# Optimization experiments

Measured on AMD Instinct MI355X. Metric: run time of the kernel, lower is better.

The kernel has to match this reference:

```python
import jax, jax.numpy as jnp
import numpy as np

N, M = 3000, 6000            # nodes, edges
FV, FE, H1, H2, NC = 128, 64, 256, 128, 16


def setup_inputs() -> dict:
    key = jax.random.key(0)
    ks = jax.random.split(key, 20)
    r = lambda i, sh: jax.random.normal(ks[i], sh, dtype=jnp.float32)
    return dict(
        X=r(0, (N, FV)),
        Z=r(1, (M, FE)),
        adj_e=jax.random.uniform(ks[2], (M, M), dtype=jnp.float32),
        adj_v=jax.random.uniform(ks[3], (N, N), dtype=jnp.float32),
        T=jax.random.uniform(ks[4], (N, M), dtype=jnp.float32),
        edge_index=jax.random.randint(ks[5], (2, 2 * M), 0, N),
        W1=r(6, (FV, H1)) * 0.05, b1=jnp.zeros((H1,), jnp.float32),
        p2=r(7, (1, H1)), W2=r(8, (FE, FE)) * 0.05, b2=jnp.zeros((FE,), jnp.float32),
        p3=r(9, (1, H1)), W3=r(10, (FE, FE)) * 0.05, b3=jnp.zeros((FE,), jnp.float32),
        p32=r(11, (1, H1)), W32=r(12, (FE, FE)) * 0.05, b32=jnp.zeros((FE,), jnp.float32),
        p4=r(13, (1, FE)), W4=r(14, (H1, H2)) * 0.05,
        b4g=jnp.zeros((H2,), jnp.float32), b4=jnp.zeros((H2,), jnp.float32),
        W5=r(15, (H2, NC)) * 0.05, b5=jnp.zeros((NC,), jnp.float32),
    )


def gcn(x, W, b, edge_index, n):
    """PyG GCNConv: symmetric-normalized A+I propagation."""
    src, dst = edge_index[0], edge_index[1]
    loop = jnp.arange(n)
    s = jnp.concatenate([src, loop])
    d = jnp.concatenate([dst, loop])
    deg = jax.ops.segment_sum(jnp.ones(s.shape[0], x.dtype), d, num_segments=n)
    dinv = jnp.where(deg > 0, jax.lax.rsqrt(deg), 0.0)
    norm = dinv[s] * dinv[d]                      # [E+n]
    xw = x @ W                                    # [n, out]
    return jax.ops.segment_sum(xw[s] * norm[:, None], d, num_segments=n) + b


def edge_layer(Hv, He, adj_e, T, p, W, b):
    # multiplier2 = T.T @ diag(Hv @ p.T) @ T, done as a fused column scale of T
    sv = (Hv @ p.T)[:, 0]                         # [n]
    m2 = T.T @ (T * sv[:, None])                  # [m, m]
    idx = jnp.arange(m2.shape[0])
    M3 = m2.at[idx, idx].set(1.0)                 # identity on diag, m2 off-diag
    A = M3 * adj_e
    An = A / A.max(axis=0, keepdims=True)         # column-max normalize
    return An @ (He @ W) + b


def reference(X, Z, adj_e, adj_v, T, edge_index,
              W1, b1, p2, W2, b2, p3, W3, b3, p32, W32, b32,
              p4, W4, b4g, b4, W5, b5):
    relu = jax.nn.relu
    # gc1: plain GCN on nodes (normalGCN=True), edges passed through
    Xh = relu(gcn(X, W1, b1, edge_index, N))
    Zh = relu(Z)
    # gc2, gc3, gc3_2: edge layers
    Zh = relu(edge_layer(Xh, Zh, adj_e, T, p2, W2, b2)); Xh = relu(Xh)
    Zh = relu(edge_layer(Xh, Zh, adj_e, T, p3, W3, b3)); Xh = relu(Xh)
    Zh = relu(edge_layer(Xh, Zh, adj_e, T, p32, W32, b32)); Xh = relu(Xh)
    # gc4: node layer with multiplier1 = T @ diag(He @ p.T) @ T.T
    se = (Zh @ p4.T)[:, 0]                        # [m]
    mult1 = (T * se[None, :]) @ T.T               # [n, n]
    X4 = mult1 @ gcn(Xh, W4, b4g, edge_index, N) + b4
    Xh = relu(X4); Zh = relu(Zh)
    # gc5: plain GCN -> softmax over classes
    X5 = gcn(Xh, W5, b5, edge_index, N)
    return jax.nn.softmax(X5, axis=1)
```

## Files before the change

### kernel.cpp

```cpp
#include <hip/hip_runtime.h>
#include <cmath>
#include <cstddef>

#define NN 3000
#define MM 6000
#define FV 128
#define FE 64
#define H1 256
#define H2 128
#define NC 16
#define E2 12000

#define CT_E 47
#define CTA_E 48
#define KT_E 94
#define CT_M 24
#define KT_M 188
#define KT_A 188
#define NPK_M 94
#define PKA_BYTES ((size_t)CTA_E * KT_E * 8192)
#define PKM_BYTES ((size_t)CT_M * KT_M * 8192)
#define APK_BYTES ((size_t)CT_E * KT_A * 8192)

static inline int cdiv(int a, int b) { return (a + b - 1) / b; }

typedef __attribute__((ext_vector_type(8))) short short8;
typedef __attribute__((ext_vector_type(4))) float f32x4;

__device__ inline void atomicMaxFloat(float* addr, float v) {
  if (v >= 0.f) atomicMax((int*)addr, __float_as_int(v));
  else          atomicMin((unsigned int*)addr, __float_as_uint(v));
}

__device__ inline unsigned short b2h(float x) {
  unsigned int u = __float_as_uint(x);
  return (unsigned short)((u + 0x7FFFu + ((u >> 16) & 1u)) >> 16);
}

__device__ inline void bsplit(float x, unsigned short& h, unsigned short& l) {
  h = b2h(x);
  float hf = __uint_as_float(((unsigned int)h) << 16);
  l = b2h(x - hf);
}

__global__ void k_fill(float* p, float v, int n) {
  int i = blockIdx.x * blockDim.x + threadIdx.x;
  if (i < n) p[i] = v;
}

__global__ void k_fill_bias(float* p, const float* __restrict__ bias, int nmask, int total) {
  int i = blockIdx.x * blockDim.x + threadIdx.x;
  if (i < total) p[i] = bias[i & nmask];
}

__global__ void k_relu_copy(const float* __restrict__ in, float* __restrict__ out, int n) {
  int i = blockIdx.x * blockDim.x + threadIdx.x;
  if (i < n) out[i] = fmaxf(in[i], 0.f);
}

__global__ void k_relu(float* p, int n) {
  int i = blockIdx.x * blockDim.x + threadIdx.x;
  if (i < n) p[i] = fmaxf(p[i], 0.f);
}

__global__ void k_deg_count(const int* __restrict__ dst, float* deg, int ne) {
  int e = blockIdx.x * blockDim.x + threadIdx.x;
  if (e < ne) atomicAdd(&deg[dst[e]], 1.f);
}

__global__ void k_dinv(float* deg, int n) {
  int i = blockIdx.x * blockDim.x + threadIdx.x;
  if (i < n) deg[i] = rsqrtf(deg[i] + 1.0f);
}

__global__ void k_gcn_init(const float* __restrict__ xw, const float* __restrict__ dinv,
                           const float* __restrict__ bias, float* __restrict__ out,
                           int n, int flog2) {
  int idx = blockIdx.x * blockDim.x + threadIdx.x;
  int F = 1 << flog2;
  if (idx < n * F) {
    int i = idx >> flog2;
    int f = idx & (F - 1);
    float di = dinv[i];
    out[idx] = xw[idx] * di * di + bias[f];
  }
}

__global__ void k_gcn_scatter(const float* __restrict__ xw, const int* __restrict__ src,
                              const int* __restrict__ dst, const float* __restrict__ dinv,
                              float* __restrict__ out, int ne, int flog2) {
  int idx = blockIdx.x * blockDim.x + threadIdx.x;
  int F = 1 << flog2;
  if (idx < ne * F) {
    int e = idx >> flog2;
    int f = idx & (F - 1);
    int s = src[e], d = dst[e];
    atomicAdd(&out[d * F + f], xw[s * F + f] * dinv[s] * dinv[d]);
  }
}

__global__ void k_rowdot(const float* __restrict__ Xv, const float* __restrict__ p,
                         float* __restrict__ out, int rows, int K) {
  int row = blockIdx.x * 4 + (threadIdx.x >> 6);
  int lane = threadIdx.x & 63;
  if (row >= rows) return;
  float acc = 0.f;
  for (int k = lane; k < K; k += 64) acc += Xv[(size_t)row * K + k] * p[k];
  for (int off = 32; off > 0; off >>= 1) acc += __shfl_xor(acc, off);
  if (lane == 0) out[row] = acc;
}

__global__ void k_prep(const float* __restrict__ HeW, const float* __restrict__ cmax,
                       const float* __restrict__ bias,
                       float* __restrict__ Bc, float* __restrict__ Zh, int total) {
  int idx = blockIdx.x * blockDim.x + threadIdx.x;
  if (idx < total) {
    Bc[idx] = HeW[idx] / cmax[idx >> 6];
    Zh[idx] = bias[idx & 63];
  }
}

__global__ void k_prep_pack(const float* __restrict__ HeW, const float* __restrict__ cmax,
                            const float* __restrict__ bias,
                            float* __restrict__ Zh, char* __restrict__ Bpk, int Kd) {
  int kt = blockIdx.x;
  int t = threadIdx.x;
  int f = t >> 2, g = t & 3;
  float bf = bias[f];
  unsigned short hv[8];
#pragma unroll
  for (int e = 0; e < 8; ++e) {
    int k = kt * 32 + g * 8 + e;
    float v = 0.f;
    if (k < Kd) {
      v = HeW[(size_t)k * 64 + f] / cmax[k];
      Zh[(size_t)k * 64 + f] = bf;
    }
    hv[e] = b2h(v);
  }
  uint4 H;
  H.x = (unsigned)hv[0] | ((unsigned)hv[1] << 16);
  H.y = (unsigned)hv[2] | ((unsigned)hv[3] << 16);
  H.z = (unsigned)hv[4] | ((unsigned)hv[5] << 16);
  H.w = (unsigned)hv[6] | ((unsigned)hv[7] << 16);
  *(uint4*)(Bpk + (size_t)kt * 4096 + f * 64 + ((g ^ ((f >> 1) & 3)) * 16)) = H;
}

__global__ void k_pack_g(const float* __restrict__ g, char* __restrict__ gpk, int Kd) {
  int kt = blockIdx.x;
  int t = threadIdx.x;
#pragma unroll
  for (int it = 0; it < 2; ++it) {
    int idx = it * 256 + t;
    int f = idx >> 2, gsw = idx & 3;
    int gq = gsw ^ ((f >> 1) & 3);
    unsigned short hv[8];
#pragma unroll
    for (int e = 0; e < 8; ++e) {
      int k = kt * 32 + gq * 8 + e;
      float v = (k < Kd) ? g[(size_t)k * 128 + f] : 0.f;
      hv[e] = b2h(v);
    }
    uint4 H;
    H.x = (unsigned)hv[0] | ((unsigned)hv[1] << 16);
    H.y = (unsigned)hv[2] | ((unsigned)hv[3] << 16);
    H.z = (unsigned)hv[4] | ((unsigned)hv[5] << 16);
    H.w = (unsigned)hv[6] | ((unsigned)hv[7] << 16);
    *(uint4*)(gpk + (size_t)kt * 8192 + idx * 16) = H;
  }
}

__global__ void k_scale_pack(const char* __restrict__ src, char* __restrict__ dst,
                             const float* __restrict__ s, float* __restrict__ cmax,
                             int nkt, int nk, int Md) {
  int ct = blockIdx.x, kt = blockIdx.y;
  size_t base = ((size_t)ct * nkt + kt) * 8192;
  int t = threadIdx.x;
  if (cmax && kt == 0 && t < 128) {
    int cc = ct * 128 + t;
    if (cc < Md) cmax[cc] = -INFINITY;
  }
#pragma unroll
  for (int it = 0; it < 2; ++it) {
    int idx = it * 256 + t;
    int c = idx >> 2, gsw = idx & 3;
    int g = gsw ^ ((c >> 1) & 3);
    uint4 H = *(const uint4*)(src + base + idx * 16);
    unsigned int hw[4] = {H.x, H.y, H.z, H.w};
    unsigned int ow[4];
#pragma unroll
    for (int p = 0; p < 4; ++p) {
      int k0 = kt * 32 + g * 8 + p * 2;
      float s0 = (k0 < nk) ? s[k0] : 0.f;
      float s1 = (k0 + 1 < nk) ? s[k0 + 1] : 0.f;
      float v0 = __uint_as_float((hw[p] & 0xFFFFu) << 16) * s0;
      float v1 = __uint_as_float((hw[p] >> 16) << 16) * s1;
      ow[p] = (unsigned)b2h(v0) | ((unsigned)b2h(v1) << 16);
    }
    uint4 O;
    O.x = ow[0]; O.y = ow[1]; O.z = ow[2]; O.w = ow[3];
    *(uint4*)(dst + base + idx * 16) = O;
  }
}

__global__ void k_pack_edge(const float* __restrict__ T, const float* __restrict__ svp,
                            char* __restrict__ ph, char* __restrict__ pl,
                            float* __restrict__ cmax,
                            int scaled, int Md, int Kd, int nkt) {
  int ct = blockIdx.x, kt = blockIdx.y;
  size_t base = ((size_t)ct * nkt + kt) * 8192;
  int t = threadIdx.x;
  if (scaled && kt == 0 && t < 128) {
    int cc = ct * 128 + t;
    if (cc < Md) cmax[cc] = -INFINITY;
  }
#pragma unroll
  for (int it = 0; it < 2; ++it) {
    int tau = it * 256 + t;
    int c = tau & 127;
    int g = tau >> 7;
    int gc = ct * 128 + c;
    int off = c * 64 + ((g ^ ((c >> 1) & 3)) * 16);
    unsigned short hv[8], lv[8];
#pragma unroll
    for (int e = 0; e < 8; ++e) {
      int k = kt * 32 + g * 8 + e;
      float v = 0.f;
      if (k < Kd && gc < Md) {
        v = T[(size_t)k * Md + gc];
        if (scaled) v *= svp[k];
      }
      bsplit(v, hv[e], lv[e]);
    }
    uint4 H, L;
    H.x = (unsigned)hv[0] | ((unsigned)hv[1] << 16);
    H.y = (unsigned)hv[2] | ((unsigned)hv[3] << 16);
    H.z = (unsigned)hv[4] | ((unsigned)hv[5] << 16);
    H.w = (unsigned)hv[6] | ((unsigned)hv[7] << 16);
    *(uint4*)(ph + base + off) = H;
    if (pl) {
      L.x = (unsigned)lv[0] | ((unsigned)lv[1] << 16);
      L.y = (unsigned)lv[2] | ((unsigned)lv[3] << 16);
      L.z = (unsigned)lv[4] | ((unsigned)lv[5] << 16);
      L.w = (unsigned)lv[6] | ((unsigned)lv[7] << 16);
      *(uint4*)(pl + base + off) = L;
    }
  }
}

__global__ void k_pack_tt(const float* __restrict__ T, const float* __restrict__ sep,
                          char* __restrict__ ph, char* __restrict__ pl,
                          int scaled, int Mt, int Kt, int nkt) {
  int ct = blockIdx.x, kt = blockIdx.y;
  size_t base = ((size_t)ct * nkt + kt) * 8192;
  int t = threadIdx.x;
#pragma unroll
  for (int it = 0; it < 2; ++it) {
    int tau = it * 256 + t;
    int c = tau >> 2;
    int g = tau & 3;
    int node = ct * 128 + c;
    int off = c * 64 + ((g ^ ((c >> 1) & 3)) * 16);
    unsigned short hv[8], lv[8];
#pragma unroll
    for (int e = 0; e < 8; ++e) {
      int k = kt * 32 + g * 8 + e;
      float v = 0.f;
      if (node < Mt && k < Kt) {
        v = T[(size_t)node * Kt + k];
        if (scaled) v *= sep[k];
      }
      bsplit(v, hv[e], lv[e]);
    }
    uint4 H, L;
    H.x = (unsigned)hv[0] | ((unsigned)hv[1] << 16);
    H.y = (unsigned)hv[2] | ((unsigned)hv[3] << 16);
    H.z = (unsigned)hv[4] | ((unsigned)hv[5] << 16);
    H.w = (unsigned)hv[6] | ((unsigned)hv[7] << 16);
    *(uint4*)(ph + base + off) = H;
    if (pl) {
      L.x = (unsigned)lv[0] | ((unsigned)lv[1] << 16);
      L.y = (unsigned)lv[2] | ((unsigned)lv[3] << 16);
      L.z = (unsigned)lv[4] | ((unsigned)lv[5] << 16);
      L.w = (unsigned)lv[6] | ((unsigned)lv[7] << 16);
      *(uint4*)(pl + base + off) = L;
    }
  }
}

template <int EPI>
__global__ __launch_bounds__(512) void k_tsvt_pk(const char* __restrict__ pAh,
                                                 const char* __restrict__ pBh,
                                                 const float* __restrict__ adj,
                                                 char* __restrict__ Opk,
                                                 float* __restrict__ cmax,
                                                 int Md, int nkt, int nbtI, int nbtJ,
                                                 int npk) {
  __shared__ __align__(16) char smem[49152];
  const int tid = threadIdx.x;
  const int lane = tid & 63;
  const int w = tid >> 6;
  const int wr = w >> 1;
  const int wc = w & 1;
  const int r16 = lane & 15;
  const int kb = lane >> 4;

  int nwg = nbtI * nbtJ;
  int orig = blockIdx.x;
  int q = nwg >> 3, r = nwg & 7;
  int xcd = orig & 7, pos = orig >> 3;
  int wgid = (xcd < r ? xcd * (q + 1) : r * (q + 1) + (xcd - r) * q) + pos;
  int gpb = 8 * nbtJ;
  int g0 = wgid / gpb;
  int rem = wgid - g0 * gpb;
  int gh = nbtI - g0 * 8; if (gh > 8) gh = 8;
  int bj = rem / gh;
  int bi = g0 * 8 + (rem - bj * gh);

  const int i0 = bi * 256, j0 = bj * 128;

  const char* srcb[3];
  srcb[0] = pAh + ((size_t)(2 * bi) * nkt) * 8192;
  srcb[1] = pAh + ((size_t)(2 * bi + 1) * nkt) * 8192;
  srcb[2] = pBh + ((size_t)bj * nkt) * 8192;
  const int woff = w * 1024 + lane * 16;

  auto stage = [&](int kt, int buf) {
#pragma unroll
    for (int rnd = 0; rnd < 3; ++rnd) {
      const char* s = srcb[rnd] + (size_t)kt * 8192 + woff;
      __builtin_amdgcn_global_load_lds(
          (const __attribute__((address_space(1))) void*)s,
          (__attribute__((address_space(3))) void*)(smem + buf * 24576 + rnd * 8192 + woff),
          16, 0, 0);
    }
  };

  f32x4 acc[4][4];
#pragma unroll
  for (int a = 0; a < 4; ++a)
#pragma unroll
    for (int b = 0; b < 4; ++b) acc[a][b] = 0.f;

  stage(0, 0);
  __syncthreads();
  int cur = 0;
  for (int kt = 0; kt < nkt; ++kt) {
    if (kt + 1 < nkt) stage(kt + 1, cur ^ 1);
    const char* sA = smem + cur * 24576;
    const char* sB = sA + 16384;

    short8 bh[4];
#pragma unroll
    for (int nj = 0; nj < 4; ++nj) {
      int col = wc * 64 + nj * 16 + r16;
      bh[nj] = *(const short8*)(sB + col * 64 + ((kb ^ ((col >> 1) & 3)) * 16));
    }
#pragma unroll
    for (int mi = 0; mi < 4; ++mi) {
      int row = wr * 64 + mi * 16 + r16;
      int off = (row >> 7) * 8192 + (row & 127) * 64 + ((kb ^ ((row >> 1) & 3)) * 16);
      short8 ah = *(const short8*)(sA + off);
#pragma unroll
      for (int nj = 0; nj < 4; ++nj)
        acc[mi][nj] = __builtin_amdgcn_mfma_f32_16x16x32_bf16(ah, bh[nj], acc[mi][nj], 0, 0, 0);
    }
    __syncthreads();
    cur ^= 1;
  }

#pragma unroll
  for (int nj = 0; nj < 4; ++nj) {
    int j = j0 + wc * 64 + nj * 16 + r16;
    float cm = -INFINITY;
    bool jok = (j < Md);
#pragma unroll
    for (int mi = 0; mi < 4; ++mi) {
      int ib = i0 + wr * 64 + mi * 16 + kb * 4;
      f32x4 a = acc[mi][nj];
#pragma unroll
      for (int r = 0; r < 4; ++r) {
        int i = ib + r;
        if (i < Md && jok) {
          float v = a[r];
          if (EPI == 1) {
            if (i == j) v = 1.0f;
            v *= __builtin_nontemporal_load(&adj[(size_t)i * Md + j]);
            cm = fmaxf(cm, v);
          }
          *(unsigned short*)(Opk + ((size_t)(i >> 7) * npk + (j >> 5)) * 8192
              + (i & 127) * 64 + ((((j >> 3) & 3) ^ ((i >> 1) & 3)) * 16) + (j & 7) * 2)
              = b2h(v);
        }
      }
    }
    if (EPI == 1) {
      cm = fmaxf(cm, __shfl_xor(cm, 16));
      cm = fmaxf(cm, __shfl_xor(cm, 32));
      if (kb == 0 && jok) atomicMaxFloat(&cmax[j], cm);
    }
  }
}

__global__ __launch_bounds__(256) void k_zh(const char* __restrict__ Apk,
                                            const char* __restrict__ Bpk,
                                            float* __restrict__ Zh,
                                            int Mn, int nktA, int zchunk) {
  __shared__ __align__(16) char smem[12288];
  const int tid = threadIdx.x;
  const int lane = tid & 63;
  const int w = tid >> 6;
  const int r16 = lane & 15;
  const int kb = lane >> 4;
  const int bi = blockIdx.x;
  const int kt0 = blockIdx.y * zchunk;
  const int kt1 = min(nktA, kt0 + zchunk);
  const int i0 = bi * 128;

  f32x4 acc[2][4];
#pragma unroll
  for (int a = 0; a < 2; ++a)
#pragma unroll
    for (int b = 0; b < 4; ++b) acc[a][b] = 0.f;

  for (int kt = kt0; kt < kt1; ++kt) {
    const char* As = Apk + ((size_t)bi * nktA + kt) * 8192;
    const char* Bs = Bpk + (size_t)kt * 4096;
    __builtin_amdgcn_global_load_lds(
        (const __attribute__((address_space(1))) void*)(As + tid * 16),
        (__attribute__((address_space(3))) void*)(smem + tid * 16), 16, 0, 0);
    __builtin_amdgcn_global_load_lds(
        (const __attribute__((address_space(1))) void*)(As + 4096 + tid * 16),
        (__attribute__((address_space(3))) void*)(smem + 4096 + tid * 16), 16, 0, 0);
    __builtin_amdgcn_global_load_lds(
        (const __attribute__((address_space(1))) void*)(Bs + tid * 16),
        (__attribute__((address_space(3))) void*)(smem + 8192 + tid * 16), 16, 0, 0);
    __syncthreads();
    short8 bh[4];
#pragma unroll
    for (int nj = 0; nj < 4; ++nj) {
      int f = nj * 16 + r16;
      bh[nj] = *(const short8*)(smem + 8192 + f * 64 + ((kb ^ ((f >> 1) & 3)) * 16));
    }
#pragma unroll
    for (int mi = 0; mi < 2; ++mi) {
      int c = w * 32 + mi * 16 + r16;
      short8 ah = *(const short8*)(smem + c * 64 + ((kb ^ ((c >> 1) & 3)) * 16));
#pragma unroll
      for (int nj = 0; nj < 4; ++nj)
        acc[mi][nj] = __builtin_amdgcn_mfma_f32_16x16x32_bf16(ah, bh[nj], acc[mi][nj], 0, 0, 0);
    }
    __syncthreads();
  }
#pragma unroll
  for (int mi = 0; mi < 2; ++mi) {
    int ib = i0 + w * 32 + mi * 16 + kb * 4;
#pragma unroll
    for (int nj = 0; nj < 4; ++nj) {
      int f = nj * 16 + r16;
      f32x4 a = acc[mi][nj];
#pragma unroll
      for (int r = 0; r < 4; ++r) {
        int i = ib + r;
        if (i < Mn) atomicAdd(&Zh[(size_t)i * 64 + f], a[r]);
      }
    }
  }
}

__global__ __launch_bounds__(256) void k_zh128(const char* __restrict__ Apk,
                                               const char* __restrict__ Bpk,
                                               float* __restrict__ C,
                                               int Mn, int nktA, int zchunk) {
  __shared__ __align__(16) char smem[16384];
  const int tid = threadIdx.x;
  const int lane = tid & 63;
  const int w = tid >> 6;
  const int r16 = lane & 15;
  const int kb = lane >> 4;
  const int bi = blockIdx.x;
  const int kt0 = blockIdx.y * zchunk;
  const int kt1 = min(nktA, kt0 + zchunk);
  const int i0 = bi * 128;

  f32x4 acc[2][8];
#pragma unroll
  for (int a = 0; a < 2; ++a)
#pragma unroll
    for (int b = 0; b < 8; ++b) acc[a][b] = 0.f;

  for (int kt = kt0; kt < kt1; ++kt) {
    const char* As = Apk + ((size_t)bi * nktA + kt) * 8192;
    const char* Bs = Bpk + (size_t)kt * 8192;
#pragma unroll
    for (int o = 0; o < 4; ++o) {
      int idx = o * 256 + tid;
      const char* s = (idx < 512) ? (As + idx * 16) : (Bs + (idx - 512) * 16);
      __builtin_amdgcn_global_load_lds(
          (const __attribute__((address_space(1))) void*)s,
          (__attribute__((address_space(3))) void*)(smem + idx * 16), 16, 0, 0);
    }
    __syncthreads();
    short8 bh[8];
#pragma unroll
    for (int nj = 0; nj < 8; ++nj) {
      int f = nj * 16 + r16;
      bh[nj] = *(const short8*)(smem + 8192 + f * 64 + ((kb ^ ((f >> 1) & 3)) * 16));
    }
#pragma unroll
    for (int mi = 0; mi < 2; ++mi) {
      int c = w * 32 + mi * 16 + r16;
      short8 ah = *(const short8*)(smem + c * 64 + ((kb ^ ((c >> 1) & 3)) * 16));
#pragma unroll
      for (int nj = 0; nj < 8; ++nj)
        acc[mi][nj] = __builtin_amdgcn_mfma_f32_16x16x32_bf16(ah, bh[nj], acc[mi][nj], 0, 0, 0);
    }
    __syncthreads();
  }
#pragma unroll
  for (int mi = 0; mi < 2; ++mi) {
    int ib = i0 + w * 32 + mi * 16 + kb * 4;
#pragma unroll
    for (int nj = 0; nj < 8; ++nj) {
      int f = nj * 16 + r16;
      f32x4 a = acc[mi][nj];
#pragma unroll
      for (int r = 0; r < 4; ++r) {
        int i = ib + r;
        if (i < Mn) atomicAdd(&C[(size_t)i * 128 + f], a[r]);
      }
    }
  }
}

template <int EPI>
__global__ __launch_bounds__(256) void k_tsvt_cvt(const float* __restrict__ Tmat,
                                                  const float* __restrict__ svp,
                                                  const float* __restrict__ adj,
                                                  float* __restrict__ Out,
                                                  float* __restrict__ cmax,
                                                  int Md, int Kd) {
  __shared__ __align__(16) unsigned short sAh[128 * 32];
  __shared__ __align__(16) unsigned short sAl[128 * 32];
  __shared__ __align__(16) unsigned short sBh[128 * 32];
  __shared__ __align__(16) unsigned short sBl[128 * 32];
  const int tid = threadIdx.x;
  const int lane = tid & 63;
  const int w = tid >> 6;
  const int wr = w >> 1, wc = w & 1;
  const int r16 = lane & 15;
  const int kb = lane >> 4;
  const int i0 = blockIdx.y * 128;
  const int j0 = blockIdx.x * 128;
  f32x4 acc[4][4];
#pragma unroll
  for (int a = 0; a < 4; ++a)
#pragma unroll
    for (int b = 0; b < 4; ++b) acc[a][b] = 0.f;
  for (int k0 = 0; k0 < Kd; k0 += 32) {
#pragma unroll
    for (int it = 0; it < 4; ++it) {
      int s = tid + it * 256;
      int ci = s & 127;
      int kq = s >> 7;
      int kk = kq * 4;
      int kbq = kq >> 1, half = kq & 1;
      int off = ci * 64 + (kbq ^ ((ci >> 1) & 3)) * 16 + half * 8;
      float va[4];
#pragma unroll
      for (int e = 0; e < 4; ++e) {
        int k = k0 + kk + e;
        int c = i0 + ci;
        va[e] = (k < Kd && c < Md) ? Tmat[(size_t)k * Md + c] : 0.f;
      }
      unsigned short h0, h1, h2, h3, l0, l1, l2, l3;
      bsplit(va[0], h0, l0); bsplit(va[1], h1, l1);
      bsplit(va[2], h2, l2); bsplit(va[3], h3, l3);
      uint2 hp, lp;
      hp.x = (unsigned)h0 | ((unsigned)h1 << 16); hp.y = (unsigned)h2 | ((unsigned)h3 << 16);
      lp.x = (unsigned)l0 | ((unsigned)l1 << 16); lp.y = (unsigned)l2 | ((unsigned)l3 << 16);
      *(uint2*)((char*)sAh + off) = hp;
      *(uint2*)((char*)sAl + off) = lp;
      float vb[4];
#pragma unroll
      for (int e = 0; e < 4; ++e) {
        int k = k0 + kk + e;
        int c = j0 + ci;
        float svv = (k < Kd) ? svp[k] : 0.f;
        vb[e] = (k < Kd && c < Md) ? Tmat[(size_t)k * Md + c] * svv : 0.f;
      }
      bsplit(vb[0], h0, l0); bsplit(vb[1], h1, l1);
      bsplit(vb[2], h2, l2); bsplit(vb[3], h3, l3);
      hp.x = (unsigned)h0 | ((unsigned)h1 << 16); hp.y = (unsigned)h2 | ((unsigned)h3 << 16);
      lp.x = (unsigned)l0 | ((unsigned)l1 << 16); lp.y = (unsigned)l2 | ((unsigned)l3 << 16);
      *(uint2*)((char*)sBh + off) = hp;
      *(uint2*)((char*)sBl + off) = lp;
    }
    __syncthreads();
    short8 bh[4], bl[4];
#pragma unroll
    for (int nj = 0; nj < 4; ++nj) {
      int col = wc * 64 + nj * 16 + r16;
      int off = col * 64 + ((kb ^ ((col >> 1) & 3)) * 16);
      bh[nj] = *(const short8*)((const char*)sBh + off);
      bl[nj] = *(const short8*)((const char*)sBl + off);
    }
#pragma unroll
    for (int mi = 0; mi < 4; ++mi) {
      int row = wr * 64 + mi * 16 + r16;
      int off = row * 64 + ((kb ^ ((row >> 1) & 3)) * 16);
      short8 ah = *(const short8*)((const char*)sAh + off);
      short8 al = *(const short8*)((const char*)sAl + off);
#pragma unroll
      for (int nj = 0; nj < 4; ++nj) {
        acc[mi][nj] = __builtin_amdgcn_mfma_f32_16x16x32_bf16(ah, bh[nj], acc[mi][nj], 0, 0, 0);
        acc[mi][nj] = __builtin_amdgcn_mfma_f32_16x16x32_bf16(ah, bl[nj], acc[mi][nj], 0, 0, 0);
        acc[mi][nj] = __builtin_amdgcn_mfma_f32_16x16x32_bf16(al, bh[nj], acc[mi][nj], 0, 0, 0);
      }
    }
    __syncthreads();
  }
#pragma unroll
  for (int nj = 0; nj < 4; ++nj) {
    int j = j0 + wc * 64 + nj * 16 + r16;
    float cm = -INFINITY;
#pragma unroll
    for (int mi = 0; mi < 4; ++mi) {
      int ib = i0 + wr * 64 + mi * 16 + kb * 4;
      f32x4 a = acc[mi][nj];
#pragma unroll
      for (int r = 0; r < 4; ++r) {
        int i = ib + r;
        if (i < Md && j < Md) {
          float v = a[r];
          if (EPI == 1) {
            if (i == j) v = 1.0f;
            v *= adj[(size_t)i * Md + j];
            Out[(size_t)i * Md + j] = v;
            cm = fmaxf(cm, v);
          } else {
            Out[(size_t)i * Md + j] = v;
          }
        }
      }
    }
    if (EPI == 1) {
      cm = fmaxf(cm, __shfl_xor(cm, 16));
      cm = fmaxf(cm, __shfl_xor(cm, 32));
      if (kb == 0 && j < Md) atomicMaxFloat(&cmax[j], cm);
    }
  }
}

template <int SPLITK, int NT>
__global__ __launch_bounds__(256) void k_gemm64(const float* __restrict__ Am,
                                                const float* __restrict__ Bm,
                                                const float* __restrict__ bias,
                                                const float* __restrict__ kscale,
                                                float* __restrict__ C,
                                                int Mn, int Nn, int Kn, int relu) {
  __shared__ float As[16][68];
  __shared__ float Bs[16][68];
  int i0 = blockIdx.y * 64, j0 = blockIdx.x * 64;
  int kchunk = (Kn + SPLITK - 1) / SPLITK;
  int ks = blockIdx.z * kchunk;
  int ke = min(Kn, ks + kchunk);
  int tid = threadIdx.x;
  int tx = tid & 15, ty = tid >> 4;
  float acc[4][4] = {};
  for (int k0 = ks; k0 < ke; k0 += 16) {
#pragma unroll
    for (int l0 = 0; l0 < 1024; l0 += 256) {
      int l = l0 + tid;
      int i = l >> 4, k = l & 15;
      float v = 0.f;
      if (i0 + i < Mn && k0 + k < ke) {
        v = NT ? __builtin_nontemporal_load(&Am[(size_t)(i0 + i) * Kn + (k0 + k)])
               : Am[(size_t)(i0 + i) * Kn + (k0 + k)];
        if (kscale) v *= kscale[k0 + k];
      }
      As[k][i] = v;
    }
#pragma unroll
    for (int l0 = 0; l0 < 1024; l0 += 256) {
      int l = l0 + tid;
      int k = l >> 6, j = l & 63;
      float v = 0.f;
      if (k0 + k < ke && j0 + j < Nn) v = Bm[(size_t)(k0 + k) * Nn + (j0 + j)];
      Bs[k][j] = v;
    }
    __syncthreads();
#pragma unroll
    for (int k = 0; k < 16; ++k) {
      const float4 av = *(const float4*)&As[k][ty * 4];
      const float4 bv = *(const float4*)&Bs[k][tx * 4];
      float a_[4] = {av.x, av.y, av.z, av.w};
      float b_[4] = {bv.x, bv.y, bv.z, bv.w};
#pragma unroll
      for (int ri = 0; ri < 4; ++ri)
#pragma unroll
        for (int rj = 0; rj < 4; ++rj)
          acc[ri][rj] = fmaf(a_[ri], b_[rj], acc[ri][rj]);
    }
    __syncthreads();
  }
#pragma unroll
  for (int ri = 0; ri < 4; ++ri) {
    int i = i0 + ty * 4 + ri;
    if (i >= Mn) continue;
#pragma unroll
    for (int rj = 0; rj < 4; ++rj) {
      int j = j0 + tx * 4 + rj;
      if (j >= Nn) continue;
      float v = acc[ri][rj];
      if (SPLITK > 1) {
        atomicAdd(&C[(size_t)i * Nn + j], v);
      } else {
        if (bias) v += bias[j];
        if (relu) v = fmaxf(v, 0.f);
        C[(size_t)i * Nn + j] = v;
      }
    }
  }
}

__global__ void k_transpose(const float* __restrict__ in, float* __restrict__ out,
                            int rows, int cols) {
  __shared__ float tile[32][33];
  int c0 = blockIdx.x * 32, r0 = blockIdx.y * 32;
  int tx = threadIdx.x & 31, tg = threadIdx.x >> 5;
  for (int rr = tg; rr < 32; rr += 8) {
    int r = r0 + rr, c = c0 + tx;
    tile[rr][tx] = (r < rows && c < cols) ? in[(size_t)r * cols + c] : 0.f;
  }
  __syncthreads();
  for (int rr = tg; rr < 32; rr += 8) {
    int c = c0 + rr, r = r0 + tx;
    if (c < cols && r < rows) out[(size_t)c * rows + r] = tile[tx][rr];
  }
}

__global__ void k_softmax16(const float* __restrict__ X5, float* __restrict__ out, int rows) {
  int r = blockIdx.x * blockDim.x + threadIdx.x;
  if (r >= rows) return;
  float v[16];
  float m = -INFINITY;
#pragma unroll
  for (int c = 0; c < 16; ++c) { v[c] = X5[r * 16 + c]; m = fmaxf(m, v[c]); }
  float s = 0.f;
#pragma unroll
  for (int c = 0; c < 16; ++c) { v[c] = expf(v[c] - m); s += v[c]; }
  float inv = 1.f / s;
#pragma unroll
  for (int c = 0; c < 16; ++c) out[r * 16 + c] = v[c] * inv;
}

extern "C" void kernel_launch(void* const* d_in, const int* in_sizes, int n_in,
                              void* d_out, int out_size, void* d_ws, size_t ws_size,
                              hipStream_t stream) {
  const float* X     = (const float*)d_in[0];
  const float* Z     = (const float*)d_in[1];
  const float* adj_e = (const float*)d_in[2];
  const float* Tm    = (const float*)d_in[4];
  const int*   ei    = (const int*)d_in[5];
  const int* src = ei;
  const int* dst = ei + E2;
  const float* W1  = (const float*)d_in[6];
  const float* b1  = (const float*)d_in[7];
  const float* p2  = (const float*)d_in[8];
  const float* W2  = (const float*)d_in[9];
  const float* b2  = (const float*)d_in[10];
  const float* p3  = (const float*)d_in[11];
  const float* W3  = (const float*)d_in[12];
  const float* b3  = (const float*)d_in[13];
  const float* p32 = (const float*)d_in[14];
  const float* W32 = (const float*)d_in[15];
  const float* b32 = (const float*)d_in[16];
  const float* p4  = (const float*)d_in[17];
  const float* W4  = (const float*)d_in[18];
  const float* b4g = (const float*)d_in[19];
  const float* b4  = (const float*)d_in[20];
  const float* W5  = (const float*)d_in[21];
  const float* b5  = (const float*)d_in[22];

  char* wsb = (char*)d_ws;
  const bool big = ws_size >= (size_t)310 * 1024 * 1024;

  char* Apk  = wsb;
  char* pAhi = wsb + APK_BYTES;
  char* pBhi = pAhi + PKA_BYTES;
  char* Bpk  = wsb + 145539072;
  char* mAhi = wsb;
  char* mBhi = mAhi + PKM_BYTES;
  char* Mpk  = wsb + 80000000;
  char* gpk  = wsb + 100000000;

  float* small = big ? (float*)(wsb + 182000000) : (float*)d_ws + 36000000;
  float* Xh   = small;
  float* xw   = small + 768000;
  float* Zh   = small + 1536000;
  float* HeW  = small + 1920000;
  float* Bc   = small + 2304000;
  float* g    = small + 2688000;
  float* sv   = small + 3072000;
  float* se   = small + 3076096;
  float* cmax = small + 3084288;
  float* dinv = small + 3090432;
  float* X5   = small + 3093504;
  float* A_fb     = (float*)d_ws;
  float* Tt_fb    = (float*)d_ws;
  float* mult1_fb = (float*)d_ws + 18000000;
  float* out  = (float*)d_out;

  auto gemm = [&](const float* Am, const float* Bm, const float* bias, const float* ksc,
                  float* C, int Mn, int Nn, int Kn, int relu, int splitk, int nt) {
    dim3 gr(cdiv(Nn, 64), cdiv(Mn, 64), splitk);
    if (splitk == 1) {
      if (nt) k_gemm64<1, 1><<<gr, 256, 0, stream>>>(Am, Bm, bias, ksc, C, Mn, Nn, Kn, relu);
      else    k_gemm64<1, 0><<<gr, 256, 0, stream>>>(Am, Bm, bias, ksc, C, Mn, Nn, Kn, relu);
    } else {
      if (nt) k_gemm64<4, 1><<<gr, 256, 0, stream>>>(Am, Bm, bias, ksc, C, Mn, Nn, Kn, relu);
      else    k_gemm64<4, 0><<<gr, 256, 0, stream>>>(Am, Bm, bias, ksc, C, Mn, Nn, Kn, relu);
    }
  };

  k_fill<<<cdiv(NN, 256), 256, 0, stream>>>(dinv, 0.f, NN);
  k_deg_count<<<cdiv(E2, 256), 256, 0, stream>>>(dst, dinv, E2);
  k_dinv<<<cdiv(NN, 256), 256, 0, stream>>>(dinv, NN);

  gemm(X, W1, nullptr, nullptr, xw, NN, H1, FV, 0, 1, 0);
  k_gcn_init<<<cdiv(NN * H1, 256), 256, 0, stream>>>(xw, dinv, b1, Xh, NN, 8);
  k_gcn_scatter<<<cdiv(E2 * H1, 256), 256, 0, stream>>>(xw, src, dst, dinv, Xh, E2, 8);
  k_relu<<<cdiv(NN * H1, 256), 256, 0, stream>>>(Xh, NN * H1);
  k_relu_copy<<<cdiv(MM * FE, 256), 256, 0, stream>>>(Z, Zh, MM * FE);

  if (big) {
    dim3 gp(CTA_E, KT_E);
    k_pack_edge<<<gp, 256, 0, stream>>>(Tm, nullptr, pAhi, nullptr, nullptr, 0, MM, NN, KT_E);
  }

  const float* ep[3] = {p2, p3, p32};
  const float* eW[3] = {W2, W3, W32};
  const float* eb[3] = {b2, b3, b32};
  for (int L = 0; L < 3; ++L) {
    k_rowdot<<<cdiv(NN, 4), 256, 0, stream>>>(Xh, ep[L], sv, NN, H1);
    gemm(Zh, eW[L], nullptr, nullptr, HeW, MM, FE, FE, 0, 1, 0);
    if (big) {
      dim3 gs(CT_E, KT_E);
      k_scale_pack<<<gs, 256, 0, stream>>>(pAhi, pBhi, sv, cmax, KT_E, NN, MM);
      int nbtI = cdiv(MM, 256), nbtJ = CT_E;
      k_tsvt_pk<1><<<nbtI * nbtJ, 512, 0, stream>>>(pAhi, pBhi, adj_e, Apk, cmax,
                                                    MM, KT_E, nbtI, nbtJ, KT_A);
      k_prep_pack<<<KT_A, 256, 0, stream>>>(HeW, cmax, eb[L], Zh, Bpk, MM);
      dim3 gz(CT_E, 8);
      k_zh<<<gz, 256, 0, stream>>>(Apk, Bpk, Zh, MM, KT_A, cdiv(KT_A, 8));
    } else {
      k_fill<<<cdiv(MM, 256), 256, 0, stream>>>(cmax, -INFINITY, MM);
      dim3 gm2(CT_E, CT_E);
      k_tsvt_cvt<1><<<gm2, 256, 0, stream>>>(Tm, sv, adj_e, A_fb, cmax, MM, NN);
      k_prep<<<cdiv(MM * FE, 256), 256, 0, stream>>>(HeW, cmax, eb[L], Bc, Zh, MM * FE);
      gemm(A_fb, Bc, nullptr, nullptr, Zh, MM, FE, MM, 0, 4, 1);
    }
    k_relu<<<cdiv(MM * FE, 256), 256, 0, stream>>>(Zh, MM * FE);
  }

  k_rowdot<<<cdiv(MM, 4), 256, 0, stream>>>(Zh, p4, se, MM, FE);
  gemm(Xh, W4, nullptr, nullptr, xw, NN, H2, H1, 0, 1, 0);
  k_gcn_init<<<cdiv(NN * H2, 256), 256, 0, stream>>>(xw, dinv, b4g, g, NN, 7);
  k_gcn_scatter<<<cdiv(E2 * H2, 256), 256, 0, stream>>>(xw, src, dst, dinv, g, E2, 7);
  if (big) {
    dim3 gp(CT_M, KT_M);
    k_pack_tt<<<gp, 256, 0, stream>>>(Tm, nullptr, mAhi, nullptr, 0, NN, MM, KT_M);
    dim3 gs(CT_M, KT_M);
    k_scale_pack<<<gs, 256, 0, stream>>>(mAhi, mBhi, se, nullptr, KT_M, MM, 0);
    int nbtI = cdiv(NN, 256), nbtJ = cdiv(NN, 128);
    k_tsvt_pk<0><<<nbtI * nbtJ, 512, 0, stream>>>(mAhi, mBhi, nullptr, Mpk, nullptr,
                                                  NN, KT_M, nbtI, nbtJ, NPK_M);
    k_pack_g<<<NPK_M, 256, 0, stream>>>(g, gpk, NN);
    k_fill_bias<<<cdiv(NN * H2, 256), 256, 0, stream>>>(Xh, b4, H2 - 1, NN * H2);
    dim3 gx(CT_M, 8);
    k_zh128<<<gx, 256, 0, stream>>>(Mpk, gpk, Xh, NN, NPK_M, cdiv(NPK_M, 8));
  } else {
    dim3 gt(cdiv(MM, 32), cdiv(NN, 32));
    k_transpose<<<gt, 256, 0, stream>>>(Tm, Tt_fb, NN, MM);
    dim3 gm1(cdiv(NN, 128), cdiv(NN, 128));
    k_tsvt_cvt<0><<<gm1, 256, 0, stream>>>(Tt_fb, se, nullptr, mult1_fb, nullptr, NN, MM);
    k_fill_bias<<<cdiv(NN * H2, 256), 256, 0, stream>>>(Xh, b4, H2 - 1, NN * H2);
    gemm(mult1_fb, g, nullptr, nullptr, Xh, NN, H2, NN, 0, 4, 0);
  }
  k_relu<<<cdiv(NN * H2, 256), 256, 0, stream>>>(Xh, NN * H2);

  gemm(Xh, W5, nullptr, nullptr, xw, NN, NC, H2, 0, 1, 0);
  k_gcn_init<<<cdiv(NN * NC, 256), 256, 0, stream>>>(xw, dinv, b5, X5, NN, 4);
  k_gcn_scatter<<<cdiv(E2 * NC, 256), 256, 0, stream>>>(xw, src, dst, dinv, X5, E2, 4);
  k_softmax16<<<cdiv(NN, 256), 256, 0, stream>>>(X5, out, NN);
}
```

Measured before the change: 1.421 ms.

## Exploit symmetry of T^T diag(s) T by computing only upper-triangular tiles

Measured after the change: 1.376 ms. 1.03x faster.

```diff
diff --git a/kernel.cpp b/kernel.cpp
--- a/kernel.cpp
+++ b/kernel.cpp
@@ -12,13 +12,12 @@
 #define E2 12000
 
 #define CT_E 47
-#define CTA_E 48
 #define KT_E 94
 #define CT_M 24
 #define KT_M 188
 #define KT_A 188
 #define NPK_M 94
-#define PKA_BYTES ((size_t)CTA_E * KT_E * 8192)
+#define PKA_BYTES ((size_t)48 * KT_E * 8192)
 #define PKM_BYTES ((size_t)CT_M * KT_M * 8192)
 #define APK_BYTES ((size_t)CT_E * KT_A * 8192)
 
@@ -289,14 +288,13 @@
 }
 
 template <int EPI>
-__global__ __launch_bounds__(512) void k_tsvt_pk(const char* __restrict__ pAh,
-                                                 const char* __restrict__ pBh,
-                                                 const float* __restrict__ adj,
-                                                 char* __restrict__ Opk,
-                                                 float* __restrict__ cmax,
-                                                 int Md, int nkt, int nbtI, int nbtJ,
-                                                 int npk) {
-  __shared__ __align__(16) char smem[49152];
+__global__ __launch_bounds__(256) void k_tsvt_sym(const char* __restrict__ pAh,
+                                                  const char* __restrict__ pBh,
+                                                  const float* __restrict__ adj,
+                                                  char* __restrict__ Opk,
+                                                  float* __restrict__ cmax,
+                                                  int Md, int nkt, int nbt, int npk) {
+  __shared__ __align__(16) char smem[32768];
   const int tid = threadIdx.x;
   const int lane = tid & 63;
   const int w = tid >> 6;
@@ -305,33 +303,30 @@
   const int r16 = lane & 15;
   const int kb = lane >> 4;
 
-  int nwg = nbtI * nbtJ;
+  int nwg = nbt * (nbt + 1) / 2;
   int orig = blockIdx.x;
   int q = nwg >> 3, r = nwg & 7;
   int xcd = orig & 7, pos = orig >> 3;
   int wgid = (xcd < r ? xcd * (q + 1) : r * (q + 1) + (xcd - r) * q) + pos;
-  int gpb = 8 * nbtJ;
-  int g0 = wgid / gpb;
-  int rem = wgid - g0 * gpb;
-  int gh = nbtI - g0 * 8; if (gh > 8) gh = 8;
-  int bj = rem / gh;
-  int bi = g0 * 8 + (rem - bj * gh);
-
-  const int i0 = bi * 256, j0 = bj * 128;
-
-  const char* srcb[3];
-  srcb[0] = pAh + ((size_t)(2 * bi) * nkt) * 8192;
-  srcb[1] = pAh + ((size_t)(2 * bi + 1) * nkt) * 8192;
-  srcb[2] = pBh + ((size_t)bj * nkt) * 8192;
-  const int woff = w * 1024 + lane * 16;
+  int bi = 0, rem = wgid;
+  while (rem >= nbt - bi) { rem -= nbt - bi; ++bi; }
+  int bj = bi + rem;
+
+  const int i0 = bi * 128, j0 = bj * 128;
+
+  const char* srcA = pAh + (size_t)bi * nkt * 8192;
+  const char* srcB = pBh + (size_t)bj * nkt * 8192;
+  const int c4 = w * 4;
 
   auto stage = [&](int kt, int buf) {
 #pragma unroll
-    for (int rnd = 0; rnd < 3; ++rnd) {
-      const char* s = srcb[rnd] + (size_t)kt * 8192 + woff;
+    for (int o = 0; o < 4; ++o) {
+      int c = c4 + o;
+      int sel = c >> 3, sub = c & 7;
+      const char* s = (sel ? srcB : srcA) + (size_t)kt * 8192 + sub * 1024 + lane * 16;
       __builtin_amdgcn_global_load_lds(
           (const __attribute__((address_space(1))) void*)s,
-          (__attribute__((address_space(3))) void*)(smem + buf * 24576 + rnd * 8192 + woff),
+          (__attribute__((address_space(3))) void*)(smem + buf * 16384 + c * 1024 + lane * 16),
           16, 0, 0);
     }
   };
@@ -347,8 +342,8 @@
   int cur = 0;
   for (int kt = 0; kt < nkt; ++kt) {
     if (kt + 1 < nkt) stage(kt + 1, cur ^ 1);
-    const char* sA = smem + cur * 24576;
-    const char* sB = sA + 16384;
+    const char* sA = smem + cur * 16384;
+    const char* sB = sA + 8192;
 
     short8 bh[4];
 #pragma unroll
@@ -359,8 +354,7 @@
 #pragma unroll
     for (int mi = 0; mi < 4; ++mi) {
       int row = wr * 64 + mi * 16 + r16;
-      int off = (row >> 7) * 8192 + (row & 127) * 64 + ((kb ^ ((row >> 1) & 3)) * 16);
-      short8 ah = *(const short8*)(sA + off);
+      short8 ah = *(const short8*)(sA + row * 64 + ((kb ^ ((row >> 1) & 3)) * 16));
 #pragma unroll
       for (int nj = 0; nj < 4; ++nj)
         acc[mi][nj] = __builtin_amdgcn_mfma_f32_16x16x32_bf16(ah, bh[nj], acc[mi][nj], 0, 0, 0);
@@ -368,6 +362,12 @@
     __syncthreads();
     cur ^= 1;
   }
+
+  float rm[4][4];
+#pragma unroll
+  for (int a = 0; a < 4; ++a)
+#pragma unroll
+    for (int b = 0; b < 4; ++b) rm[a][b] = -INFINITY;
 
 #pragma unroll
   for (int nj = 0; nj < 4; ++nj) {
@@ -379,18 +379,38 @@
       int ib = i0 + wr * 64 + mi * 16 + kb * 4;
       f32x4 a = acc[mi][nj];
 #pragma unroll
-      for (int r = 0; r < 4; ++r) {
-        int i = ib + r;
-        if (i < Md && jok) {
-          float v = a[r];
+      for (int rr = 0; rr < 4; ++rr) {
+        int i = ib + rr;
+        if (i < Md && jok && i <= j) {
+          float v = a[rr];
           if (EPI == 1) {
-            if (i == j) v = 1.0f;
-            v *= __builtin_nontemporal_load(&adj[(size_t)i * Md + j]);
-            cm = fmaxf(cm, v);
+            if (i < j) {
+              float a1 = v * __builtin_nontemporal_load(&adj[(size_t)i * Md + j]);
+              *(unsigned short*)(Opk + ((size_t)(i >> 7) * npk + (j >> 5)) * 8192
+                  + (i & 127) * 64 + ((((j >> 3) & 3) ^ ((i >> 1) & 3)) * 16) + (j & 7) * 2)
+                  = b2h(a1);
+              cm = fmaxf(cm, a1);
+              float a2 = v * __builtin_nontemporal_load(&adj[(size_t)j * Md + i]);
+              *(unsigned short*)(Opk + ((size_t)(j >> 7) * npk + (i >> 5)) * 8192
+                  + (j & 127) * 64 + ((((i >> 3) & 3) ^ ((j >> 1) & 3)) * 16) + (i & 7) * 2)
+                  = b2h(a2);
+              rm[mi][rr] = fmaxf(rm[mi][rr], a2);
+            } else {
+              float a1 = __builtin_nontemporal_load(&adj[(size_t)i * Md + j]);
+              *(unsigned short*)(Opk + ((size_t)(i >> 7) * npk + (j >> 5)) * 8192
+                  + (i & 127) * 64 + ((((j >> 3) & 3) ^ ((i >> 1) & 3)) * 16) + (j & 7) * 2)
+                  = b2h(a1);
+              cm = fmaxf(cm, a1);
+            }
+          } else {
+            *(unsigned short*)(Opk + ((size_t)(i >> 7) * npk + (j >> 5)) * 8192
+                + (i & 127) * 64 + ((((j >> 3) & 3) ^ ((i >> 1) & 3)) * 16) + (j & 7) * 2)
+                = b2h(v);
+            if (i < j)
+              *(unsigned short*)(Opk + ((size_t)(j >> 7) * npk + (i >> 5)) * 8192
+                  + (j & 127) * 64 + ((((i >> 3) & 3) ^ ((j >> 1) & 3)) * 16) + (i & 7) * 2)
+                  = b2h(v);
           }
-          *(unsigned short*)(Opk + ((size_t)(i >> 7) * npk + (j >> 5)) * 8192
-              + (i & 127) * 64 + ((((j >> 3) & 3) ^ ((i >> 1) & 3)) * 16) + (j & 7) * 2)
-              = b2h(v);
         }
       }
     }
@@ -398,6 +418,21 @@
       cm = fmaxf(cm, __shfl_xor(cm, 16));
       cm = fmaxf(cm, __shfl_xor(cm, 32));
       if (kb == 0 && jok) atomicMaxFloat(&cmax[j], cm);
+    }
+  }
+  if (EPI == 1) {
+#pragma unroll
+    for (int mi = 0; mi < 4; ++mi) {
+#pragma unroll
+      for (int rr = 0; rr < 4; ++rr) {
+        float m = rm[mi][rr];
+        m = fmaxf(m, __shfl_xor(m, 1));
+        m = fmaxf(m, __shfl_xor(m, 2));
+        m = fmaxf(m, __shfl_xor(m, 4));
+        m = fmaxf(m, __shfl_xor(m, 8));
+        int i = i0 + wr * 64 + mi * 16 + kb * 4 + rr;
+        if (r16 == 0 && i < Md && m > -INFINITY) atomicMaxFloat(&cmax[i], m);
+      }
     }
   }
 }
@@ -835,22 +870,22 @@
   k_relu_copy<<<cdiv(MM * FE, 256), 256, 0, stream>>>(Z, Zh, MM * FE);
 
   if (big) {
-    dim3 gp(CTA_E, KT_E);
+    dim3 gp(CT_E, KT_E);
     k_pack_edge<<<gp, 256, 0, stream>>>(Tm, nullptr, pAhi, nullptr, nullptr, 0, MM, NN, KT_E);
   }
 
   const float* ep[3] = {p2, p3, p32};
   const float* eW[3] = {W2, W3, W32};
   const float* eb[3] = {b2, b3, b32};
+  const int ntriE = CT_E * (CT_E + 1) / 2;
   for (int L = 0; L < 3; ++L) {
     k_rowdot<<<cdiv(NN, 4), 256, 0, stream>>>(Xh, ep[L], sv, NN, H1);
     gemm(Zh, eW[L], nullptr, nullptr, HeW, MM, FE, FE, 0, 1, 0);
     if (big) {
       dim3 gs(CT_E, KT_E);
       k_scale_pack<<<gs, 256, 0, stream>>>(pAhi, pBhi, sv, cmax, KT_E, NN, MM);
-      int nbtI = cdiv(MM, 256), nbtJ = CT_E;
-      k_tsvt_pk<1><<<nbtI * nbtJ, 512, 0, stream>>>(pAhi, pBhi, adj_e, Apk, cmax,
-                                                    MM, KT_E, nbtI, nbtJ, KT_A);
+      k_tsvt_sym<1><<<ntriE, 256, 0, stream>>>(pAhi, pBhi, adj_e, Apk, cmax,
+                                               MM, KT_E, CT_E, KT_A);
       k_prep_pack<<<KT_A, 256, 0, stream>>>(HeW, cmax, eb[L], Zh, Bpk, MM);
       dim3 gz(CT_E, 8);
       k_zh<<<gz, 256, 0, stream>>>(Apk, Bpk, Zh, MM, KT_A, cdiv(KT_A, 8));
@@ -873,9 +908,9 @@
     k_pack_tt<<<gp, 256, 0, stream>>>(Tm, nullptr, mAhi, nullptr, 0, NN, MM, KT_M);
     dim3 gs(CT_M, KT_M);
     k_scale_pack<<<gs, 256, 0, stream>>>(mAhi, mBhi, se, nullptr, KT_M, MM, 0);
-    int nbtI = cdiv(NN, 256), nbtJ = cdiv(NN, 128);
-    k_tsvt_pk<0><<<nbtI * nbtJ, 512, 0, stream>>>(mAhi, mBhi, nullptr, Mpk, nullptr,
-                                                  NN, KT_M, nbtI, nbtJ, NPK_M);
+    const int ntriM = CT_M * (CT_M + 1) / 2;
+    k_tsvt_sym<0><<<ntriM, 256, 0, stream>>>(mAhi, mBhi, nullptr, Mpk, nullptr,
+                                             NN, KT_M, CT_M, NPK_M);
     k_pack_g<<<NPK_M, 256, 0, stream>>>(g, gpk, NN);
     k_fill_bias<<<cdiv(NN * H2, 256), 256, 0, stream>>>(Xh, b4, H2 - 1, NN * H2);
     dim3 gx(CT_M, 8);
```
